# Performance work log

Measured on AMD Instinct MI355X. Metric: run time of the kernel, lower is better.

## Reference

```python
import jax, jax.numpy as jnp
import numpy as np

NUM_NODES = 50000
NUM_EDGES = 800000
NUM_LABEL_EDGES = 100000
F_IN, F_HID, F_OUT = 128, 128, 64


def gcn_conv(x, src, dst, W, b, n):
    # PyG GCNConv: h = x @ W; add self-loops; symmetric normalization
    # deg counted on destination (col), including self-loop (+1).
    h = x @ W
    deg = jax.ops.segment_sum(jnp.ones(src.shape, h.dtype), dst, num_segments=n) + 1.0
    dinv = jax.lax.rsqrt(deg)  # deg >= 1 always (self-loop)
    norm = dinv[src] * dinv[dst]                       # [E]
    agg = jax.ops.segment_sum(h[src] * norm[:, None], dst, num_segments=n)
    agg = agg + h * (dinv * dinv)[:, None]             # self-loop term dinv[i]^2 * h[i]
    return agg + b


def setup_inputs() -> dict:
    key = jax.random.key(0)
    ks = jax.random.split(key, 9)
    x = jax.random.normal(ks[0], (NUM_NODES, F_IN), dtype=jnp.float32)
    edge_index = jax.random.randint(ks[1], (2, NUM_EDGES), 0, NUM_NODES, dtype=jnp.int64)
    edge_label_index = jax.random.randint(ks[2], (2, NUM_LABEL_EDGES), 0, NUM_NODES, dtype=jnp.int64)
    def glorot(k, fi, fo):
        s = (6.0 / (fi + fo)) ** 0.5
        return jax.random.uniform(k, (fi, fo), jnp.float32, -s, s)
    return {
        "x": x,
        "edge_index": edge_index,
        "edge_label_index": edge_label_index,
        "W1": glorot(ks[3], F_IN, F_HID),  "b1": jnp.zeros((F_HID,), jnp.float32),
        "W2": glorot(ks[4], F_HID, F_HID), "b2": jnp.zeros((F_HID,), jnp.float32),
        "W3": glorot(ks[5], F_HID, F_OUT), "b3": jnp.zeros((F_OUT,), jnp.float32),
    }


def reference(x, edge_index, edge_label_index, W1, b1, W2, b2, W3, b3):
    src, dst = edge_index[0], edge_index[1]
    z = jax.nn.relu(gcn_conv(x, src, dst, W1, b1, NUM_NODES))
    z = jax.nn.relu(gcn_conv(z, src, dst, W2, b2, NUM_NODES))
    z = gcn_conv(z, src, dst, W3, b3, NUM_NODES)
    # decode: dot product of endpoint embeddings per label edge
    return jnp.sum(z[edge_label_index[0]] * z[edge_label_index[1]], axis=-1)
```

## Files before the change

### kernel.cpp

```cpp
#include <hip/hip_runtime.h>
#include <hip/hip_bf16.h>
#include <stdint.h>

#define NN 50000
#define NE 800000
#define NL 100000
#define SLOTS 64

#define NB 196
#define BSH 8
#define BCAP 5376

typedef __attribute__((ext_vector_type(8))) short bf16x8;
typedef __attribute__((ext_vector_type(4))) float f32x4;
typedef __attribute__((ext_vector_type(4))) unsigned int u32x4;
typedef __attribute__((ext_vector_type(8))) unsigned short u16x8;

__device__ __forceinline__ float asf(unsigned int u) {
    union { unsigned int i; float f; } c; c.i = u; return c.f;
}
__device__ __forceinline__ float bflo(unsigned int x) { return asf(x << 16); }
__device__ __forceinline__ float bfhi(unsigned int x) { return asf(x & 0xffff0000u); }
__device__ __forceinline__ unsigned short f2bf(float f) {
    union { float f; unsigned int i; } c; c.f = f;
    unsigned int u = c.i + (0x7fffu + ((c.i >> 16) & 1u));
    return (unsigned short)(u >> 16);
}

__global__ void k_wprep(const float* __restrict__ W1, const float* __restrict__ W2,
                        const float* __restrict__ W3, unsigned short* __restrict__ Wt,
                        int* __restrict__ cursor) {
    int idx = blockIdx.x * 256 + threadIdx.x;
    if (idx < NB) cursor[idx] = 0;
    const float* W; unsigned short* O; int base, Mloc;
    if (idx < 16384)      { W = W1; O = Wt;         base = idx;         Mloc = 128; }
    else if (idx < 32768) { W = W2; O = Wt + 16384; base = idx - 16384; Mloc = 128; }
    else                  { W = W3; O = Wt + 32768; base = idx - 32768; Mloc = 64;  }
    int n = base >> 7, k = base & 127;
    O[base] = f2bf(W[k * Mloc + n]);
}

__global__ __launch_bounds__(256) void k_bin(
        const int* __restrict__ src, const int* __restrict__ dst,
        int* __restrict__ cursor, unsigned int* __restrict__ binbuf) {
    __shared__ int hcnt[NB];
    __shared__ int hbase[NB];
    __shared__ unsigned int epk[2048];
    int tid = threadIdx.x;
    if (tid < NB) hcnt[tid] = 0;
    __syncthreads();
    int e0 = blockIdx.x * 2048;
    int e1 = min(e0 + 2048, NE);
    for (int e = e0 + tid; e < e1; e += 256) {
        int d = dst[e], s = src[e];
        atomicAdd(&hcnt[d >> BSH], 1);
        epk[e - e0] = (unsigned int)s | ((unsigned int)d << 16);
    }
    __syncthreads();
    if (tid < NB) { hbase[tid] = atomicAdd(&cursor[tid], hcnt[tid]); hcnt[tid] = 0; }
    __syncthreads();
    for (int e = e0 + tid; e < e1; e += 256) {
        unsigned int pk = epk[e - e0];
        int b = (int)(pk >> 16) >> BSH;
        int p = hbase[b] + atomicAdd(&hcnt[b], 1);
        if (p < BCAP)
            __builtin_nontemporal_store(pk, &binbuf[(size_t)b * BCAP + p]);
    }
}

__global__ __launch_bounds__(256) void k_csr(
        const unsigned int* __restrict__ binbuf, const int* __restrict__ cursor,
        int* __restrict__ deg, unsigned short* __restrict__ colp) {
    __shared__ unsigned short lcol[256 * SLOTS];
    __shared__ int ldeg[256];
    int tid = threadIdx.x;
    int blk = blockIdx.x;
    int base = blk << BSH;
    int nNodes = min(256, NN - base);
    ldeg[tid] = 0;
    u32x4* lz = (u32x4*)lcol;
#pragma unroll
    for (int i = 0; i < 8; ++i) lz[i * 256 + tid] = (u32x4){0, 0, 0, 0};
    __syncthreads();
    int cnt = min(cursor[blk], BCAP);
    for (int e = tid; e < cnt; e += 256) {
        unsigned int pk = __builtin_nontemporal_load(&binbuf[(size_t)blk * BCAP + e]);
        int d = (int)(pk >> 16) - base;
        int p = atomicAdd(&ldeg[d], 1);
        if (p < SLOTS) lcol[d * SLOTS + p] = (unsigned short)(pk & 0xffffu);
    }
    __syncthreads();
    if (tid < nNodes) deg[base + tid] = ldeg[tid];
    u32x4* gout = (u32x4*)(colp + (size_t)base * SLOTS);
    const u32x4* lin = (const u32x4*)lcol;
    for (int i = tid; i < nNodes * 8; i += 256) gout[i] = lin[i];
}

__global__ __launch_bounds__(256) void k_gemm1(
        const float* __restrict__ A, const unsigned short* __restrict__ Wt,
        const int* __restrict__ deg, unsigned short* __restrict__ Outb, int N) {
    constexpr int K = 128;
    constexpr int NT = 8;
    int tid = threadIdx.x;
    int lane = tid & 63, wave = tid >> 6;
    int m = lane & 15, quad = lane >> 4;
    int rowA = blockIdx.x * 64 + wave * 16 + m;
    int rA = min(rowA, N - 1);

    bf16x8 afr[4];
    const float* p = A + (size_t)rA * K + quad * 8;
#pragma unroll
    for (int s = 0; s < 4; ++s) {
        float4 lo = *(const float4*)(p + s * 32);
        float4 hi = *(const float4*)(p + s * 32 + 4);
        bf16x8 r;
        r[0] = (short)f2bf(lo.x); r[1] = (short)f2bf(lo.y);
        r[2] = (short)f2bf(lo.z); r[3] = (short)f2bf(lo.w);
        r[4] = (short)f2bf(hi.x); r[5] = (short)f2bf(hi.y);
        r[6] = (short)f2bf(hi.z); r[7] = (short)f2bf(hi.w);
        afr[s] = r;
    }

    f32x4 acc[NT];
#pragma unroll
    for (int t = 0; t < NT; ++t) { acc[t][0] = 0.f; acc[t][1] = 0.f; acc[t][2] = 0.f; acc[t][3] = 0.f; }
#pragma unroll
    for (int t = 0; t < NT; ++t) {
        const unsigned short* wp = Wt + (size_t)(t * 16 + m) * K + quad * 8;
#pragma unroll
        for (int s = 0; s < 4; ++s) {
            bf16x8 bfr = *(const bf16x8*)(wp + s * 32);
            acc[t] = __builtin_amdgcn_mfma_f32_16x16x32_bf16(afr[s], bfr, acc[t], 0, 0, 0);
        }
    }

    int outRowBase = blockIdx.x * 64 + wave * 16 + quad * 4;
    float di[4];
#pragma unroll
    for (int i = 0; i < 4; ++i) di[i] = rsqrtf((float)deg[min(outRowBase + i, N - 1)] + 1.0f);
#pragma unroll
    for (int t = 0; t < NT; ++t)
#pragma unroll
        for (int i = 0; i < 4; ++i) {
            int rr = outRowBase + i;
            if (rr < N) Outb[(size_t)rr * 128 + t * 16 + m] = f2bf(acc[t][i] * di[i]);
        }
}

template <int M_>
__global__ __launch_bounds__(256) void k_agg_gemm(
        const unsigned short* __restrict__ hs, const int* __restrict__ deg,
        const unsigned short* __restrict__ colp, const float* __restrict__ bias,
        const unsigned short* __restrict__ Wt, unsigned short* __restrict__ Outb) {
    constexpr int K = 128;
    constexpr int NT = M_ / 64;
    __shared__ __align__(16) unsigned short As[16][136];
    int tid = threadIdx.x;
    int lane = tid & 63, wave = tid >> 6;
    int tileBase = blockIdx.x * 16;
    int g = lane >> 4, c = lane & 15;
    const unsigned short* hc = hs + c * 8;
    int nodeB = tileBase + wave * 4;

    float bv[8];
    {
        const float4* bp = (const float4*)(bias + c * 8);
        float4 b0 = bp[0], b1 = bp[1];
        bv[0] = b0.x; bv[1] = b0.y; bv[2] = b0.z; bv[3] = b0.w;
        bv[4] = b1.x; bv[5] = b1.y; bv[6] = b1.z; bv[7] = b1.w;
    }

    int cnt[4];
    u16x8 sl[4];
#pragma unroll
    for (int t = 0; t < 4; ++t) cnt[t] = min(deg[nodeB + t], SLOTS);
#pragma unroll
    for (int t = 0; t < 4; ++t)
        sl[t] = *(const u16x8*)(colp + (size_t)(nodeB + t) * SLOTS + g * 8);

    unsigned int smk = (g == 0) ? 0xffffffffu : 0u;

#pragma unroll
    for (int t = 0; t < 4; ++t) {
        int r = wave * 4 + t;
        int node = nodeB + t;

        u32x4 sv = *(const u32x4*)(hc + (size_t)node * K);
        u32x4 vv[8];
        unsigned int mk[8];
#pragma unroll
        for (int k2 = 0; k2 < 8; ++k2) {
            int slot = g * 8 + k2;
            mk[k2] = (slot < cnt[t]) ? 0xffffffffu : 0u;
            vv[k2] = *(const u32x4*)(hc + (size_t)(int)sl[t][k2] * K);
        }

        float acc[8];
#pragma unroll
        for (int k = 0; k < 4; ++k) {
            unsigned int xv = sv[k] & smk;
            acc[2 * k] = bflo(xv); acc[2 * k + 1] = bfhi(xv);
        }
#pragma unroll
        for (int k2 = 0; k2 < 8; ++k2) {
#pragma unroll
            for (int k = 0; k < 4; ++k) {
                unsigned int xv = vv[k2][k] & mk[k2];
                acc[2 * k] += bflo(xv); acc[2 * k + 1] += bfhi(xv);
            }
        }

        if (cnt[t] > 32) {
            int mi = (lane < cnt[t]) ? (int)colp[(size_t)node * SLOTS + lane] : 0;
            for (int j = 32; j < cnt[t]; j += 4) {
                int i0 = __shfl(mi, j + g, 64);
                u32x4 v0 = {0, 0, 0, 0};
                if (j + g < cnt[t]) v0 = *(const u32x4*)(hc + (size_t)i0 * K);
#pragma unroll
                for (int k = 0; k < 4; ++k) {
                    acc[2 * k] += bflo(v0[k]); acc[2 * k + 1] += bfhi(v0[k]);
                }
            }
        }

#pragma unroll
        for (int k = 0; k < 8; ++k) {
            acc[k] += __shfl_xor(acc[k], 16, 64);
            acc[k] += __shfl_xor(acc[k], 32, 64);
        }
        if (g == 0) {
            float di = rsqrtf((float)cnt[t] + 1.0f);
            u32x4 pv;
#pragma unroll
            for (int k = 0; k < 4; ++k) {
                float o0 = fmaxf(di * acc[2 * k]     + bv[2 * k],     0.f);
                float o1 = fmaxf(di * acc[2 * k + 1] + bv[2 * k + 1], 0.f);
                pv[k] = (unsigned int)f2bf(o0) | ((unsigned int)f2bf(o1) << 16);
            }
            *(u32x4*)&As[r][c * 8] = pv;
        }
    }
    __syncthreads();

    int m = lane & 15, quad = lane >> 4;
    bf16x8 afr[4];
#pragma unroll
    for (int s = 0; s < 4; ++s)
        afr[s] = *(const bf16x8*)&As[m][s * 32 + quad * 8];

    f32x4 gacc[NT];
#pragma unroll
    for (int t = 0; t < NT; ++t) { gacc[t][0] = 0.f; gacc[t][1] = 0.f; gacc[t][2] = 0.f; gacc[t][3] = 0.f; }
#pragma unroll
    for (int t = 0; t < NT; ++t) {
        int ct = wave * NT + t;
        const unsigned short* wp = Wt + (size_t)(ct * 16 + m) * K + quad * 8;
#pragma unroll
        for (int s = 0; s < 4; ++s) {
            bf16x8 bfr = *(const bf16x8*)(wp + s * 32);
            gacc[t] = __builtin_amdgcn_mfma_f32_16x16x32_bf16(afr[s], bfr, gacc[t], 0, 0, 0);
        }
    }

    int rowBase = tileBase + quad * 4;
    float di[4];
#pragma unroll
    for (int i = 0; i < 4; ++i) di[i] = rsqrtf((float)deg[rowBase + i] + 1.0f);
#pragma unroll
    for (int t = 0; t < NT; ++t) {
        int ct = wave * NT + t;
#pragma unroll
        for (int i = 0; i < 4; ++i)
            Outb[(size_t)(rowBase + i) * M_ + ct * 16 + m] = f2bf(gacc[t][i] * di[i]);
    }
}

__global__ __launch_bounds__(256) void k_agg64(
        const unsigned short* __restrict__ hs, const int* __restrict__ deg,
        const unsigned short* __restrict__ colp, const float* __restrict__ bias,
        unsigned short* __restrict__ out, int n) {
    int tid = threadIdx.x;
    int wave = tid >> 6, lane = tid & 63;
    int node = blockIdx.x * 4 + wave;
    int g = lane >> 3, c = lane & 7;
    const unsigned short* hc = hs + c * 8;

    int cnt = min(deg[node], SLOTS);
    u16x8 sl = *(const u16x8*)(colp + (size_t)node * SLOTS + g * 8);

    u32x4 sv = *(const u32x4*)(hc + (size_t)node * 64);
    u32x4 vv[8];
    unsigned int mk[8];
#pragma unroll
    for (int k2 = 0; k2 < 8; ++k2) {
        int slot = g * 8 + k2;
        mk[k2] = (slot < cnt) ? 0xffffffffu : 0u;
        vv[k2] = *(const u32x4*)(hc + (size_t)(int)sl[k2] * 64);
    }

    unsigned int smk = (g == 0) ? 0xffffffffu : 0u;
    float acc[8];
#pragma unroll
    for (int k = 0; k < 4; ++k) {
        unsigned int xv = sv[k] & smk;
        acc[2 * k] = bflo(xv); acc[2 * k + 1] = bfhi(xv);
    }
#pragma unroll
    for (int k2 = 0; k2 < 8; ++k2) {
#pragma unroll
        for (int k = 0; k < 4; ++k) {
            unsigned int xv = vv[k2][k] & mk[k2];
            acc[2 * k] += bflo(xv); acc[2 * k + 1] += bfhi(xv);
        }
    }
#pragma unroll
    for (int k = 0; k < 8; ++k) {
        acc[k] += __shfl_xor(acc[k], 8, 64);
        acc[k] += __shfl_xor(acc[k], 16, 64);
        acc[k] += __shfl_xor(acc[k], 32, 64);
    }
    if (g == 0) {
        float di = rsqrtf((float)cnt + 1.0f);
        const float4* bp = (const float4*)(bias + c * 8);
        float4 b0 = bp[0], b1 = bp[1];
        float bb[8] = {b0.x, b0.y, b0.z, b0.w, b1.x, b1.y, b1.z, b1.w};
        u32x4 pv;
#pragma unroll
        for (int k = 0; k < 4; ++k) {
            float o0 = di * acc[2 * k]     + bb[2 * k];
            float o1 = di * acc[2 * k + 1] + bb[2 * k + 1];
            pv[k] = (unsigned int)f2bf(o0) | ((unsigned int)f2bf(o1) << 16);
        }
        *(u32x4*)(out + (size_t)node * 64 + c * 8) = pv;
    }
}

__global__ __launch_bounds__(256) void k_decode(
        const unsigned short* __restrict__ z, const int* __restrict__ ls,
        const int* __restrict__ ld, float* __restrict__ out, int nl) {
    int tid = threadIdx.x;
    int lane = tid & 63, wave = tid >> 6;
    int g = lane >> 3, c = lane & 7;
    int e = (blockIdx.x * 4 + wave) * 4 + (g >> 1);
    int row = (g & 1) ? ld[e] : ls[e];
    u32x4 v = *(const u32x4*)(z + (size_t)row * 64 + c * 8);
    u32x4 w;
#pragma unroll
    for (int k = 0; k < 4; ++k) w[k] = (unsigned int)__shfl_xor((int)v[k], 8, 64);
    float p = 0.f;
#pragma unroll
    for (int k = 0; k < 4; ++k)
        p += bflo(v[k]) * bflo(w[k]) + bfhi(v[k]) * bfhi(w[k]);
    p += __shfl_xor(p, 1, 64);
    p += __shfl_xor(p, 2, 64);
    p += __shfl_xor(p, 4, 64);
    if ((lane & 15) == 0) out[e] = p;
}


static inline size_t align256(size_t x) { return (x + 255) & ~(size_t)255; }

extern "C" void kernel_launch(void* const* d_in, const int* in_sizes, int n_in,
                              void* d_out, int out_size, void* d_ws, size_t ws_size,
                              hipStream_t stream) {
    const float* x  = (const float*)d_in[0];
    const int*   ei = (const int*)d_in[1];
    const int*   li = (const int*)d_in[2];
    const float* W1 = (const float*)d_in[3];
    const float* b1 = (const float*)d_in[4];
    const float* W2 = (const float*)d_in[5];
    const float* b2 = (const float*)d_in[6];
    const float* W3 = (const float*)d_in[7];
    const float* b3 = (const float*)d_in[8];
    float* out = (float*)d_out;

    const int* src = ei;
    const int* dst = ei + NE;
    const int* ls = li;
    const int* ld = li + NL;

    char* ws = (char*)d_ws;
    size_t off = 0;
    int* deg    = (int*)(ws + off); off += align256(NN * 4);
    int* cursor = (int*)(ws + off); off += align256(NB * 4);
    unsigned int* binbuf = (unsigned int*)(ws + off); off += align256((size_t)NB * BCAP * 4);
    unsigned short* colp = (unsigned short*)(ws + off); off += align256((size_t)NN * SLOTS * 2);
    unsigned short* Wtb  = (unsigned short*)(ws + off); off += align256(40960 * 2);
    unsigned short* bufA = (unsigned short*)(ws + off); off += align256((size_t)NN * 128 * 2);
    unsigned short* bufB = (unsigned short*)(ws + off); off += align256((size_t)NN * 128 * 2);
    unsigned short* bufZ = (unsigned short*)(ws + off); off += align256((size_t)NN * 64 * 2);

    k_wprep<<<160, 256, 0, stream>>>(W1, W2, W3, Wtb, cursor);
    k_bin<<<391, 256, 0, stream>>>(src, dst, cursor, binbuf);
    k_csr<<<NB, 256, 0, stream>>>(binbuf, cursor, deg, colp);

    k_gemm1<<<782, 256, 0, stream>>>(x, Wtb, deg, bufA, NN);
    k_agg_gemm<128><<<3125, 256, 0, stream>>>(bufA, deg, colp, b1, Wtb + 16384, bufB);
    k_agg_gemm<64><<<3125, 256, 0, stream>>>(bufB, deg, colp, b2, Wtb + 32768, bufA);
    k_agg64<<<12500, 256, 0, stream>>>(bufA, deg, colp, b3, bufZ, NN);
    k_decode<<<6250, 256, 0, stream>>>(bufZ, ls, ld, out, NL);
}
```

Measured before the change: 240.6 us.

## Interleave neighbor slots and split gathers into degree-gated halves for occupancy

The bucketing kernel now stores the first 32 neighbor slots interleaved so that each 16-lane group holds neighbors 4*k2+g. The aggregation kernels then load only the first 16 neighbor rows unconditionally and fetch the next 16 only when degree exceeds 16. This cuts live registers and wasted gathers for low-degree nodes, and launch bounds request 8 waves-per-SIMD occupancy. k_agg64 is reworked to use 16 lanes of 4 features each, gains the >32 overflow path, and uses the real degree for normalization instead of the clamped count. Risks include register spills under the tighter launch bound and the extra branch divergence.

```diff
diff --git a/kernel.cpp b/kernel.cpp
--- a/kernel.cpp
+++ b/kernel.cpp
@@ -14,6 +14,7 @@
 typedef __attribute__((ext_vector_type(8))) short bf16x8;
 typedef __attribute__((ext_vector_type(4))) float f32x4;
 typedef __attribute__((ext_vector_type(4))) unsigned int u32x4;
+typedef __attribute__((ext_vector_type(2))) unsigned int u32x2;
 typedef __attribute__((ext_vector_type(8))) unsigned short u16x8;
 
 __device__ __forceinline__ float asf(unsigned int u) {
@@ -87,7 +88,10 @@
         unsigned int pk = __builtin_nontemporal_load(&binbuf[(size_t)blk * BCAP + e]);
         int d = (int)(pk >> 16) - base;
         int p = atomicAdd(&ldeg[d], 1);
-        if (p < SLOTS) lcol[d * SLOTS + p] = (unsigned short)(pk & 0xffffu);
+        if (p < SLOTS) {
+            int pp = (p < 32) ? ((p & 3) * 8 + (p >> 2)) : p;
+            lcol[d * SLOTS + pp] = (unsigned short)(pk & 0xffffu);
+        }
     }
     __syncthreads();
     if (tid < nNodes) deg[base + tid] = ldeg[tid];
@@ -148,7 +152,7 @@
 }
 
 template <int M_>
-__global__ __launch_bounds__(256) void k_agg_gemm(
+__global__ __launch_bounds__(256, 8) void k_agg_gemm(
         const unsigned short* __restrict__ hs, const int* __restrict__ deg,
         const unsigned short* __restrict__ colp, const float* __restrict__ bias,
         const unsigned short* __restrict__ Wt, unsigned short* __restrict__ Outb) {
@@ -162,22 +166,11 @@
     const unsigned short* hc = hs + c * 8;
     int nodeB = tileBase + wave * 4;
 
-    float bv[8];
-    {
-        const float4* bp = (const float4*)(bias + c * 8);
-        float4 b0 = bp[0], b1 = bp[1];
-        bv[0] = b0.x; bv[1] = b0.y; bv[2] = b0.z; bv[3] = b0.w;
-        bv[4] = b1.x; bv[5] = b1.y; bv[6] = b1.z; bv[7] = b1.w;
-    }
-
-    int cnt[4];
-    u16x8 sl[4];
-#pragma unroll
-    for (int t = 0; t < 4; ++t) cnt[t] = min(deg[nodeB + t], SLOTS);
-#pragma unroll
-    for (int t = 0; t < 4; ++t)
-        sl[t] = *(const u16x8*)(colp + (size_t)(nodeB + t) * SLOTS + g * 8);
-
+    int degv[4], cnt[4];
+#pragma unroll
+    for (int t = 0; t < 4; ++t) { degv[t] = deg[nodeB + t]; cnt[t] = min(degv[t], SLOTS); }
+
+    u16x8 sl = *(const u16x8*)(colp + (unsigned)nodeB * SLOTS + g * 8);
     unsigned int smk = (g == 0) ? 0xffffffffu : 0u;
 
 #pragma unroll
@@ -185,15 +178,13 @@
         int r = wave * 4 + t;
         int node = nodeB + t;
 
-        u32x4 sv = *(const u32x4*)(hc + (size_t)node * K);
-        u32x4 vv[8];
-        unsigned int mk[8];
-#pragma unroll
-        for (int k2 = 0; k2 < 8; ++k2) {
-            int slot = g * 8 + k2;
-            mk[k2] = (slot < cnt[t]) ? 0xffffffffu : 0u;
-            vv[k2] = *(const u32x4*)(hc + (size_t)(int)sl[t][k2] * K);
-        }
+        u32x4 sv = *(const u32x4*)(hc + (unsigned)node * K);
+        u32x4 vv[4];
+#pragma unroll
+        for (int k2 = 0; k2 < 4; ++k2)
+            vv[k2] = *(const u32x4*)(hc + (unsigned)sl[k2] * K);
+        u16x8 sln = sl;
+        if (t < 3) sln = *(const u16x8*)(colp + (unsigned)(node + 1) * SLOTS + g * 8);
 
         float acc[8];
 #pragma unroll
@@ -202,26 +193,41 @@
             acc[2 * k] = bflo(xv); acc[2 * k + 1] = bfhi(xv);
         }
 #pragma unroll
-        for (int k2 = 0; k2 < 8; ++k2) {
+        for (int k2 = 0; k2 < 4; ++k2) {
+            unsigned int mk = (4 * k2 + g < cnt[t]) ? 0xffffffffu : 0u;
 #pragma unroll
             for (int k = 0; k < 4; ++k) {
-                unsigned int xv = vv[k2][k] & mk[k2];
+                unsigned int xv = vv[k2][k] & mk;
                 acc[2 * k] += bflo(xv); acc[2 * k + 1] += bfhi(xv);
             }
         }
-
+        if (cnt[t] > 16) {
+#pragma unroll
+            for (int k2 = 0; k2 < 4; ++k2)
+                vv[k2] = *(const u32x4*)(hc + (unsigned)sl[k2 + 4] * K);
+#pragma unroll
+            for (int k2 = 0; k2 < 4; ++k2) {
+                unsigned int mk = (16 + 4 * k2 + g < cnt[t]) ? 0xffffffffu : 0u;
+#pragma unroll
+                for (int k = 0; k < 4; ++k) {
+                    unsigned int xv = vv[k2][k] & mk;
+                    acc[2 * k] += bflo(xv); acc[2 * k + 1] += bfhi(xv);
+                }
+            }
+        }
         if (cnt[t] > 32) {
-            int mi = (lane < cnt[t]) ? (int)colp[(size_t)node * SLOTS + lane] : 0;
+            int mi = (lane < cnt[t]) ? (int)colp[(unsigned)node * SLOTS + lane] : 0;
             for (int j = 32; j < cnt[t]; j += 4) {
                 int i0 = __shfl(mi, j + g, 64);
                 u32x4 v0 = {0, 0, 0, 0};
-                if (j + g < cnt[t]) v0 = *(const u32x4*)(hc + (size_t)i0 * K);
+                if (j + g < cnt[t]) v0 = *(const u32x4*)(hc + (unsigned)i0 * K);
 #pragma unroll
                 for (int k = 0; k < 4; ++k) {
                     acc[2 * k] += bflo(v0[k]); acc[2 * k + 1] += bfhi(v0[k]);
                 }
             }
         }
+        sl = sln;
 
 #pragma unroll
         for (int k = 0; k < 8; ++k) {
@@ -229,12 +235,15 @@
             acc[k] += __shfl_xor(acc[k], 32, 64);
         }
         if (g == 0) {
-            float di = rsqrtf((float)cnt[t] + 1.0f);
+            float di = rsqrtf((float)degv[t] + 1.0f);
+            const float4* bp = (const float4*)(bias + c * 8);
+            float4 b0 = bp[0], b1 = bp[1];
+            float bb[8] = {b0.x, b0.y, b0.z, b0.w, b1.x, b1.y, b1.z, b1.w};
             u32x4 pv;
 #pragma unroll
             for (int k = 0; k < 4; ++k) {
-                float o0 = fmaxf(di * acc[2 * k]     + bv[2 * k],     0.f);
-                float o1 = fmaxf(di * acc[2 * k + 1] + bv[2 * k + 1], 0.f);
+                float o0 = fmaxf(di * acc[2 * k]     + bb[2 * k],     0.f);
+                float o1 = fmaxf(di * acc[2 * k + 1] + bb[2 * k + 1], 0.f);
                 pv[k] = (unsigned int)f2bf(o0) | ((unsigned int)f2bf(o1) << 16);
             }
             *(u32x4*)&As[r][c * 8] = pv;
@@ -275,63 +284,82 @@
     }
 }
 
-__global__ __launch_bounds__(256) void k_agg64(
+__global__ __launch_bounds__(256, 8) void k_agg64(
         const unsigned short* __restrict__ hs, const int* __restrict__ deg,
         const unsigned short* __restrict__ colp, const float* __restrict__ bias,
         unsigned short* __restrict__ out, int n) {
     int tid = threadIdx.x;
     int wave = tid >> 6, lane = tid & 63;
     int node = blockIdx.x * 4 + wave;
-    int g = lane >> 3, c = lane & 7;
-    const unsigned short* hc = hs + c * 8;
-
-    int cnt = min(deg[node], SLOTS);
-    u16x8 sl = *(const u16x8*)(colp + (size_t)node * SLOTS + g * 8);
-
-    u32x4 sv = *(const u32x4*)(hc + (size_t)node * 64);
-    u32x4 vv[8];
-    unsigned int mk[8];
-#pragma unroll
-    for (int k2 = 0; k2 < 8; ++k2) {
-        int slot = g * 8 + k2;
-        mk[k2] = (slot < cnt) ? 0xffffffffu : 0u;
-        vv[k2] = *(const u32x4*)(hc + (size_t)(int)sl[k2] * 64);
-    }
+    int g = lane >> 4, c = lane & 15;
+    const unsigned short* hc = hs + c * 4;
+
+    int degv = deg[node];
+    int cnt = min(degv, SLOTS);
+    u16x8 sl = *(const u16x8*)(colp + (unsigned)node * SLOTS + g * 8);
+
+    u32x2 sv = *(const u32x2*)(hc + (unsigned)node * 64);
+    u32x2 vv[4];
+#pragma unroll
+    for (int k2 = 0; k2 < 4; ++k2)
+        vv[k2] = *(const u32x2*)(hc + (unsigned)sl[k2] * 64);
 
     unsigned int smk = (g == 0) ? 0xffffffffu : 0u;
-    float acc[8];
-#pragma unroll
-    for (int k = 0; k < 4; ++k) {
+    float acc[4];
+#pragma unroll
+    for (int k = 0; k < 2; ++k) {
         unsigned int xv = sv[k] & smk;
         acc[2 * k] = bflo(xv); acc[2 * k + 1] = bfhi(xv);
     }
 #pragma unroll
-    for (int k2 = 0; k2 < 8; ++k2) {
-#pragma unroll
-        for (int k = 0; k < 4; ++k) {
-            unsigned int xv = vv[k2][k] & mk[k2];
+    for (int k2 = 0; k2 < 4; ++k2) {
+        unsigned int mk = (4 * k2 + g < cnt) ? 0xffffffffu : 0u;
+#pragma unroll
+        for (int k = 0; k < 2; ++k) {
+            unsigned int xv = vv[k2][k] & mk;
             acc[2 * k] += bflo(xv); acc[2 * k + 1] += bfhi(xv);
         }
     }
-#pragma unroll
-    for (int k = 0; k < 8; ++k) {
-        acc[k] += __shfl_xor(acc[k], 8, 64);
+    if (cnt > 16) {
+#pragma unroll
+        for (int k2 = 0; k2 < 4; ++k2)
+            vv[k2] = *(const u32x2*)(hc + (unsigned)sl[k2 + 4] * 64);
+#pragma unroll
+        for (int k2 = 0; k2 < 4; ++k2) {
+            unsigned int mk = (16 + 4 * k2 + g < cnt) ? 0xffffffffu : 0u;
+#pragma unroll
+            for (int k = 0; k < 2; ++k) {
+                unsigned int xv = vv[k2][k] & mk;
+                acc[2 * k] += bflo(xv); acc[2 * k + 1] += bfhi(xv);
+            }
+        }
+    }
+    if (cnt > 32) {
+        int mi = (lane < cnt) ? (int)colp[(unsigned)node * SLOTS + lane] : 0;
+        for (int j = 32; j < cnt; j += 4) {
+            int i0 = __shfl(mi, j + g, 64);
+            u32x2 v0 = {0, 0};
+            if (j + g < cnt) v0 = *(const u32x2*)(hc + (unsigned)i0 * 64);
+#pragma unroll
+            for (int k = 0; k < 2; ++k) {
+                acc[2 * k] += bflo(v0[k]); acc[2 * k + 1] += bfhi(v0[k]);
+            }
+        }
+    }
+#pragma unroll
+    for (int k = 0; k < 4; ++k) {
         acc[k] += __shfl_xor(acc[k], 16, 64);
         acc[k] += __shfl_xor(acc[k], 32, 64);
     }
     if (g == 0) {
-        float di = rsqrtf((float)cnt + 1.0f);
-        const float4* bp = (const float4*)(bias + c * 8);
-        float4 b0 = bp[0], b1 = bp[1];
-        float bb[8] = {b0.x, b0.y, b0.z, b0.w, b1.x, b1.y, b1.z, b1.w};
-        u32x4 pv;
-#pragma unroll
-        for (int k = 0; k < 4; ++k) {
-            float o0 = di * acc[2 * k]     + bb[2 * k];
-            float o1 = di * acc[2 * k + 1] + bb[2 * k + 1];
-            pv[k] = (unsigned int)f2bf(o0) | ((unsigned int)f2bf(o1) << 16);
-        }
-        *(u32x4*)(out + (size_t)node * 64 + c * 8) = pv;
+        float di = rsqrtf((float)degv + 1.0f);
+        float4 bb = *(const float4*)(bias + c * 4);
+        u32x2 pv;
+        pv[0] = (unsigned int)f2bf(di * acc[0] + bb.x) |
+                ((unsigned int)f2bf(di * acc[1] + bb.y) << 16);
+        pv[1] = (unsigned int)f2bf(di * acc[2] + bb.z) |
+                ((unsigned int)f2bf(di * acc[3] + bb.w) << 16);
+        *(u32x2*)(out + (size_t)node * 64 + c * 4) = pv;
     }
 }
 
```

Measured after the change: 251.2 us. +4.4%, slower.
